# Performance work log

Measured on AMD Instinct MI355X. Metric: run time of the kernel, lower is better.

Reference implementation:

```python
import jax, jax.numpy as jnp
import numpy as np

N = 50000   # total nodes
D = 128     # feature dim
E = 800000  # edges (avg degree 16)
G = 100     # graphs (500 nodes each)


def setup_inputs() -> dict:
    key = jax.random.key(0)
    ks = jax.random.split(key, 9)
    s = 1.0 / np.sqrt(D)
    X = jax.random.normal(ks[0], (N, D), jnp.float32)
    src = jax.random.randint(ks[1], (E,), 0, N)
    dst = jax.random.randint(ks[2], (E,), 0, N)
    edge_index = jnp.stack([src, dst])  # [2, E]
    edge_weight = jax.random.uniform(ks[3], (E,), jnp.float32)
    # 100 graphs of 500 nodes each (graph_sizes = [500]*100)
    segment_ids = jnp.repeat(jnp.arange(G), N // G)
    return {
        "X": X,
        "edge_weight": edge_weight,
        "W1": jax.random.normal(ks[4], (D, D), jnp.float32) * s,
        "b1": jnp.zeros((D,), jnp.float32),
        "W2": jax.random.normal(ks[5], (D, D), jnp.float32) * s,
        "b2": jnp.zeros((D,), jnp.float32),
        "Wf": jax.random.normal(ks[6], (D, 1), jnp.float32) * s,
        "bf": jnp.zeros((1,), jnp.float32),
        "edge_index": edge_index,
        "segment_ids": segment_ids,
    }


def gcn_conv(X, edge_index, edge_weight, W, b):
    # h_v = sum_{(u->v)} w_e * (X @ W)[u] + b   (sparse A @ XW)
    h = X @ W                                   # [N, d_out]
    msgs = h[edge_index[0]] * edge_weight[:, None]  # [E, d_out]
    agg = jax.ops.segment_sum(msgs, edge_index[1], num_segments=N)
    return agg + b


def reference(X, edge_weight, W1, b1, W2, b2, Wf, bf, edge_index, segment_ids):
    # layer stack: conv -> relu -> dropout(eval=identity)
    h = jax.nn.relu(gcn_conv(X, edge_index, edge_weight, W1, b1))
    h = jax.nn.relu(gcn_conv(h, edge_index, edge_weight, W2, b2))
    out = jax.nn.sigmoid(gcn_conv(h, edge_index, edge_weight, Wf, bf))  # [N, 1]
    # fused per-graph mean readout (replaces split(graph_sizes) python loop)
    sums = jax.ops.segment_sum(out.sum(axis=1), segment_ids, num_segments=G)
    counts = jax.ops.segment_sum(jnp.ones((N,), out.dtype), segment_ids, num_segments=G)
    return sums / (counts * out.shape[1])  # [G]
```

## Files before the change

### kernel.cpp

```cpp
#include <hip/hip_runtime.h>
#include <hip/hip_fp16.h>

#define N_NODES 50000
#define DIM 128
#define NEDGE 800000
#define NGRAPH 100
#define NPG 500
#define NBUCKET 250
#define NPB 200
#define BCAP 4096
#define CHUNK 2048
#define EPT (CHUNK / 256)

typedef _Float16 f16x8 __attribute__((ext_vector_type(8)));
typedef float f32x4 __attribute__((ext_vector_type(4)));
typedef float f32x2 __attribute__((ext_vector_type(2)));

__device__ inline float wgt(unsigned p) {
    return __half2float(__ushort_as_half((unsigned short)(p & 0xffffu)));
}
__device__ inline void accrow(uint2 q, float w, float* acc) {
    f32x2 f;
    f = __builtin_amdgcn_cvt_pk_f32_fp8((int)q.x, false); acc[0] = fmaf(w, f[0], acc[0]); acc[1] = fmaf(w, f[1], acc[1]);
    f = __builtin_amdgcn_cvt_pk_f32_fp8((int)q.x, true);  acc[2] = fmaf(w, f[0], acc[2]); acc[3] = fmaf(w, f[1], acc[3]);
    f = __builtin_amdgcn_cvt_pk_f32_fp8((int)q.y, false); acc[4] = fmaf(w, f[0], acc[4]); acc[5] = fmaf(w, f[1], acc[5]);
    f = __builtin_amdgcn_cvt_pk_f32_fp8((int)q.y, true);  acc[6] = fmaf(w, f[0], acc[6]); acc[7] = fmaf(w, f[1], acc[7]);
}
__device__ inline unsigned pack_fp8x4(float a, float b, float c, float d) {
    int v = __builtin_amdgcn_cvt_pk_fp8_f32(a, b, 0, false);
    v = __builtin_amdgcn_cvt_pk_fp8_f32(c, d, v, true);
    return (unsigned)v;
}

__global__ void prep(const float* __restrict__ W1, const float* __restrict__ W2,
                     _Float16* __restrict__ fragW1, _Float16* __restrict__ fragW2,
                     int* __restrict__ gCur) {
    const int b = blockIdx.x;
    if (b == 128) {
        int t = threadIdx.x;
        if (t < NBUCKET) gCur[t] = t * BCAP;
        return;
    }
    const float* W = (b < 64) ? W1 : W2;
    _Float16* F = (b < 64) ? fragW1 : fragW2;
    int idx = (b & 63) * 256 + threadIdx.x;
    int j = idx & 7, l = (idx >> 3) & 63, kt = (idx >> 9) & 3, nt = idx >> 11;
    int k = kt * 32 + ((l >> 4) << 3) + j;
    int col = (nt << 4) + (l & 15);
    F[idx] = (_Float16)W[k * DIM + col];
}

__global__ void bucket_scatter(const int* __restrict__ src, const int* __restrict__ dst,
                               const float* __restrict__ w, int* __restrict__ gCur,
                               uint2* __restrict__ stage, int E) {
    __shared__ int hist[NBUCKET];
    __shared__ int base[NBUCKET];
    for (int i = threadIdx.x; i < NBUCKET; i += 256) hist[i] = 0;
    __syncthreads();
    const int e0 = blockIdx.x * CHUNK;
    int myDst[EPT];
#pragma unroll
    for (int j = 0; j < EPT; ++j) {
        int e = e0 + j * 256 + threadIdx.x;
        int d = (e < E) ? dst[e] : -1;
        myDst[j] = d;
        if (d >= 0) atomicAdd(&hist[d / NPB], 1);
    }
    __syncthreads();
    for (int i = threadIdx.x; i < NBUCKET; i += 256)
        base[i] = atomicAdd(&gCur[i], hist[i]);
    __syncthreads();
#pragma unroll
    for (int j = 0; j < EPT; ++j) {
        int d = myDst[j];
        if (d >= 0) {
            int e = e0 + j * 256 + threadIdx.x;
            int b = d / NPB;
            int p = atomicAdd(&base[b], 1);
            unsigned short wh = __half_as_ushort(__float2half_rn(w[e]));
            stage[p] = make_uint2(((unsigned)src[e] << 16) | (unsigned)wh,
                                  (unsigned)(d - b * NPB));
        }
    }
}

__device__ inline f16x8 load_afrag_f32(const float* a) {
    float4 u0 = *(const float4*)a;
    float4 u1 = *(const float4*)(a + 4);
    f16x8 r;
    r[0] = (_Float16)u0.x; r[1] = (_Float16)u0.y; r[2] = (_Float16)u0.z; r[3] = (_Float16)u0.w;
    r[4] = (_Float16)u1.x; r[5] = (_Float16)u1.y; r[6] = (_Float16)u1.z; r[7] = (_Float16)u1.w;
    return r;
}
__device__ inline f16x8 load_afrag_fp8(const unsigned char* a) {
    uint2 q = *(const uint2*)a;
    f32x2 f0 = __builtin_amdgcn_cvt_pk_f32_fp8((int)q.x, false);
    f32x2 f1 = __builtin_amdgcn_cvt_pk_f32_fp8((int)q.x, true);
    f32x2 f2 = __builtin_amdgcn_cvt_pk_f32_fp8((int)q.y, false);
    f32x2 f3 = __builtin_amdgcn_cvt_pk_f32_fp8((int)q.y, true);
    f16x8 r;
    r[0] = (_Float16)f0[0]; r[1] = (_Float16)f0[1]; r[2] = (_Float16)f1[0]; r[3] = (_Float16)f1[1];
    r[4] = (_Float16)f2[0]; r[5] = (_Float16)f2[1]; r[6] = (_Float16)f3[0]; r[7] = (_Float16)f3[1];
    return r;
}

template <typename TIN>
__device__ inline void gemm_tile(const TIN* __restrict__ A, const _Float16* fragW,
                                 unsigned char* __restrict__ C, int blk, int tid) {
    const int lane = tid & 63;
    const int wid = tid >> 6;
    const int row0 = blk * 128 + wid * 16;
    if (row0 >= N_NODES) return;
    const int arow = row0 + (lane & 15);
    const int koff = (lane >> 4) << 3;
    f32x4 acc[8] = {};
#pragma unroll
    for (int kt = 0; kt < 4; ++kt) {
        f16x8 a;
        const TIN* ap = A + (size_t)arow * DIM + kt * 32 + koff;
        if constexpr (sizeof(TIN) == 4) a = load_afrag_f32((const float*)ap);
        else                            a = load_afrag_fp8((const unsigned char*)ap);
#pragma unroll
        for (int nt = 0; nt < 8; ++nt) {
            f16x8 b = *(const f16x8*)&fragW[(((nt << 2) | kt) << 9) | (lane << 3)];
            acc[nt] = __builtin_amdgcn_mfma_f32_16x16x32_f16(a, b, acc[nt], 0, 0, 0);
        }
    }
    const int crow = row0 + ((lane >> 4) << 2);
    const int ccol = lane & 15;
#pragma unroll
    for (int nt = 0; nt < 8; ++nt) {
#pragma unroll
        for (int r = 0; r < 4; ++r) {
            int v8 = __builtin_amdgcn_cvt_pk_fp8_f32(acc[nt][r], acc[nt][r], 0, false);
            C[(size_t)(crow + r) * DIM + (nt << 4) + ccol] = (unsigned char)(v8 & 0xff);
        }
    }
}

template <typename TIN>
__global__ __launch_bounds__(512) void gemm_mfma(const TIN* __restrict__ A,
                                                 const _Float16* __restrict__ fragWg,
                                                 unsigned char* __restrict__ C) {
    __shared__ __align__(16) _Float16 fragW[16384];
    const int tid = threadIdx.x;
    for (int i = tid; i < 2048; i += 512)
        ((uint4*)fragW)[i] = ((const uint4*)fragWg)[i];
    __syncthreads();
    gemm_tile<TIN>(A, fragW, C, blockIdx.x, tid);
}

#define MFMA_BLK ((N_NODES + 127) / 128)
__global__ __launch_bounds__(512) void gemm1_build(
        const float* __restrict__ A, const _Float16* __restrict__ fragWg,
        unsigned char* __restrict__ C, const int* __restrict__ gCur,
        const uint2* __restrict__ stage, unsigned int* __restrict__ pack,
        int2* __restrict__ range) {
    __shared__ __align__(16) _Float16 fragW[16384];
    __shared__ int lhist[NPB];
    __shared__ int lincl[256];
    __shared__ int lcur[NPB];
    const int tid = threadIdx.x;
    if (blockIdx.x < MFMA_BLK) {
        for (int i = tid; i < 2048; i += 512)
            ((uint4*)fragW)[i] = ((const uint4*)fragWg)[i];
        __syncthreads();
        gemm_tile<float>(A, fragW, C, blockIdx.x, tid);
        return;
    }
    const int b = blockIdx.x - MFMA_BLK;
    const int t = tid;
    const int cnt = gCur[b] - b * BCAP;
    for (int i = t; i < NPB; i += 512) lhist[i] = 0;
    __syncthreads();
    unsigned myX[BCAP / 512];
    int myLd[BCAP / 512];
#pragma unroll
    for (int j = 0; j < BCAP / 512; ++j) {
        int i = j * 512 + t;
        if (i < cnt) {
            uint2 r = stage[b * BCAP + i];
            myX[j] = r.x;
            myLd[j] = (int)r.y;
            atomicAdd(&lhist[r.y], 1);
        } else {
            myLd[j] = -1;
        }
    }
    __syncthreads();
    int h = (t < NPB) ? lhist[t] : 0;
    if (t < 256) lincl[t] = h;
    __syncthreads();
    for (int off = 1; off < 256; off <<= 1) {
        int v = (t >= off && t < 256) ? lincl[t - off] : 0;
        __syncthreads();
        if (t < 256) lincl[t] += v;
        __syncthreads();
    }
    if (t < NPB) lcur[t] = lincl[t] - h;
    __syncthreads();
#pragma unroll
    for (int j = 0; j < BCAP / 512; ++j) {
        if (myLd[j] >= 0) {
            int p = atomicAdd(&lcur[myLd[j]], 1);
            pack[b * BCAP + p] = myX[j];
        }
    }
    if (t < NPB) {
        int v = b * NPB + t;
        range[v] = make_int2(b * BCAP + lincl[t] - h, b * BCAP + lincl[t]);
    }
}

template <int MODE>
__global__ void gather_feat(const unsigned char* __restrict__ msg,
                            const unsigned int* __restrict__ pack,
                            const int2* __restrict__ range, const float* __restrict__ bias,
                            const float* __restrict__ wf, unsigned char* __restrict__ outF,
                            float* __restrict__ outS) {
    int gid = blockIdx.x * blockDim.x + threadIdx.x;
    int grp = gid >> 4, lane = gid & 15;
    if (grp >= N_NODES) return;
    int2 r = range[grp];
    int beg = r.x, end = r.y;
    float acc[8] = {};
    int i = beg;
    for (; i + 7 < end; i += 8) {
        unsigned p[8];
        uint2 q[8];
#pragma unroll
        for (int j = 0; j < 8; ++j) p[j] = pack[i + j];
#pragma unroll
        for (int j = 0; j < 8; ++j)
            q[j] = ((const uint2*)(msg + (size_t)(p[j] >> 16) * DIM))[lane];
#pragma unroll
        for (int j = 0; j < 8; ++j) accrow(q[j], wgt(p[j]), acc);
    }
    for (; i + 3 < end; i += 4) {
        unsigned p0 = pack[i], p1 = pack[i + 1], p2 = pack[i + 2], p3 = pack[i + 3];
        uint2 q0 = ((const uint2*)(msg + (size_t)(p0 >> 16) * DIM))[lane];
        uint2 q1 = ((const uint2*)(msg + (size_t)(p1 >> 16) * DIM))[lane];
        uint2 q2 = ((const uint2*)(msg + (size_t)(p2 >> 16) * DIM))[lane];
        uint2 q3 = ((const uint2*)(msg + (size_t)(p3 >> 16) * DIM))[lane];
        accrow(q0, wgt(p0), acc);
        accrow(q1, wgt(p1), acc);
        accrow(q2, wgt(p2), acc);
        accrow(q3, wgt(p3), acc);
    }
    for (; i < end; ++i) {
        unsigned p = pack[i];
        uint2 q = ((const uint2*)(msg + (size_t)(p >> 16) * DIM))[lane];
        accrow(q, wgt(p), acc);
    }
    float4 b0 = ((const float4*)bias)[2 * lane];
    float4 b1 = ((const float4*)bias)[2 * lane + 1];
    acc[0] = fmaxf(acc[0] + b0.x, 0.f); acc[1] = fmaxf(acc[1] + b0.y, 0.f);
    acc[2] = fmaxf(acc[2] + b0.z, 0.f); acc[3] = fmaxf(acc[3] + b0.w, 0.f);
    acc[4] = fmaxf(acc[4] + b1.x, 0.f); acc[5] = fmaxf(acc[5] + b1.y, 0.f);
    acc[6] = fmaxf(acc[6] + b1.z, 0.f); acc[7] = fmaxf(acc[7] + b1.w, 0.f);
    if (MODE == 0) {
        uint2 o;
        o.x = pack_fp8x4(acc[0], acc[1], acc[2], acc[3]);
        o.y = pack_fp8x4(acc[4], acc[5], acc[6], acc[7]);
        ((uint2*)(outF + (size_t)grp * DIM))[lane] = o;
    } else {
        float4 f0 = ((const float4*)wf)[2 * lane];
        float4 f1 = ((const float4*)wf)[2 * lane + 1];
        float d = acc[0] * f0.x + acc[1] * f0.y + acc[2] * f0.z + acc[3] * f0.w
                + acc[4] * f1.x + acc[5] * f1.y + acc[6] * f1.z + acc[7] * f1.w;
#pragma unroll
        for (int off = 8; off; off >>= 1) d += __shfl_down(d, off, 16);
        if (lane == 0) outS[grp] = d;
    }
}

__global__ void final_readout(const float* __restrict__ s, const unsigned int* __restrict__ pack,
                              const int2* __restrict__ range, const float* __restrict__ bfp,
                              float* __restrict__ out) {
    __shared__ float red[256];
    int g = blockIdx.x;
    float bf = bfp[0];
    float sum = 0.f;
    for (int n = threadIdx.x; n < NPG; n += blockDim.x) {
        int v = g * NPG + n;
        int2 r = range[v];
        float a = 0.f;
        for (int i = r.x; i < r.y; ++i) {
            unsigned int p = pack[i];
            a += wgt(p) * s[p >> 16];
        }
        a += bf;
        sum += 1.f / (1.f + expf(-a));
    }
    red[threadIdx.x] = sum;
    __syncthreads();
    for (int t = 128; t > 0; t >>= 1) {
        if (threadIdx.x < t) red[threadIdx.x] += red[threadIdx.x + t];
        __syncthreads();
    }
    if (threadIdx.x == 0) out[g] = red[0] / (float)NPG;
}

extern "C" void kernel_launch(void* const* d_in, const int* in_sizes, int n_in,
                              void* d_out, int out_size, void* d_ws, size_t ws_size,
                              hipStream_t stream) {
    const float* X  = (const float*)d_in[0];
    const float* ew = (const float*)d_in[1];
    const float* W1 = (const float*)d_in[2];
    const float* b1 = (const float*)d_in[3];
    const float* W2 = (const float*)d_in[4];
    const float* b2 = (const float*)d_in[5];
    const float* Wf = (const float*)d_in[6];
    const float* bf = (const float*)d_in[7];
    const int* ei   = (const int*)d_in[8];
    const int* src  = ei;
    const int* dst  = ei + NEDGE;

    float* out = (float*)d_out;

    char* ws = (char*)d_ws;
    size_t off = 0;
    unsigned char* bufA = (unsigned char*)(ws + off); off += (size_t)N_NODES * DIM;
    unsigned char* bufB = (unsigned char*)(ws + off); off += (size_t)N_NODES * DIM;
    uint2* stage = (uint2*)(ws + off);  off += (size_t)NBUCKET * BCAP * 8;
    unsigned int* pack = (unsigned int*)(ws + off); off += (size_t)NBUCKET * BCAP * 4;
    int2* range = (int2*)(ws + off);    off += (size_t)N_NODES * 8;
    int* gCur   = (int*)(ws + off);     off += (size_t)256 * 4;
    _Float16* fragW1 = (_Float16*)(ws + off); off += (size_t)16384 * 2;
    _Float16* fragW2 = (_Float16*)(ws + off); off += (size_t)16384 * 2;
    float* s_node = (float*)(ws + off); off += (size_t)N_NODES * 4;

    const int TB = 256;
    const int SCAT_BLK = (NEDGE + CHUNK - 1) / CHUNK;
    const int GATHER_BLK = (N_NODES * 16 + TB - 1) / TB;

    prep<<<129, TB, 0, stream>>>(W1, W2, fragW1, fragW2, gCur);
    bucket_scatter<<<SCAT_BLK, TB, 0, stream>>>(src, dst, ew, gCur, stage, NEDGE);
    gemm1_build<<<MFMA_BLK + NBUCKET, 512, 0, stream>>>(X, fragW1, bufA, gCur,
                                                        stage, pack, range);
    gather_feat<0><<<GATHER_BLK, TB, 0, stream>>>(bufA, pack, range, b1,
                                                  nullptr, bufB, nullptr);
    gemm_mfma<unsigned char><<<MFMA_BLK, 512, 0, stream>>>(bufB, fragW2, bufA);
    gather_feat<1><<<GATHER_BLK, TB, 0, stream>>>(bufA, pack, range, b2,
                                                  Wf, nullptr, s_node);
    final_readout<<<NGRAPH, TB, 0, stream>>>(s_node, pack, range, bf, out);
}
```

Measured before the change: 106.9 us.

## Fuse layer-1 gather with layer-2 GEMM via shared-memory fp16 tile

Each 256-thread block now gathers 16 destination nodes for layer 1 and writes the bias+ReLU result as fp16 into a swizzled LDS tile. It then runs MFMA against W2 straight from that tile, with each of four waves producing two 16-column tiles. This removes a kernel launch, the fp8 round trip of the intermediate hidden features through global memory, and the fp8 dequant in the A-fragment load. The intermediate is now kept in fp16 rather than fp8, which changes precision slightly. fragW2 is read from global memory rather than staged in LDS, and each block does only a small GEMM.

```diff
diff --git a/kernel.cpp b/kernel.cpp
--- a/kernel.cpp
+++ b/kernel.cpp
@@ -92,21 +92,9 @@
     r[4] = (_Float16)u1.x; r[5] = (_Float16)u1.y; r[6] = (_Float16)u1.z; r[7] = (_Float16)u1.w;
     return r;
 }
-__device__ inline f16x8 load_afrag_fp8(const unsigned char* a) {
-    uint2 q = *(const uint2*)a;
-    f32x2 f0 = __builtin_amdgcn_cvt_pk_f32_fp8((int)q.x, false);
-    f32x2 f1 = __builtin_amdgcn_cvt_pk_f32_fp8((int)q.x, true);
-    f32x2 f2 = __builtin_amdgcn_cvt_pk_f32_fp8((int)q.y, false);
-    f32x2 f3 = __builtin_amdgcn_cvt_pk_f32_fp8((int)q.y, true);
-    f16x8 r;
-    r[0] = (_Float16)f0[0]; r[1] = (_Float16)f0[1]; r[2] = (_Float16)f1[0]; r[3] = (_Float16)f1[1];
-    r[4] = (_Float16)f2[0]; r[5] = (_Float16)f2[1]; r[6] = (_Float16)f3[0]; r[7] = (_Float16)f3[1];
-    return r;
-}
-
-template <typename TIN>
-__device__ inline void gemm_tile(const TIN* __restrict__ A, const _Float16* fragW,
-                                 unsigned char* __restrict__ C, int blk, int tid) {
+
+__device__ inline void gemm_tile_f32(const float* __restrict__ A, const _Float16* fragW,
+                                     unsigned char* __restrict__ C, int blk, int tid) {
     const int lane = tid & 63;
     const int wid = tid >> 6;
     const int row0 = blk * 128 + wid * 16;
@@ -116,10 +104,7 @@
     f32x4 acc[8] = {};
 #pragma unroll
     for (int kt = 0; kt < 4; ++kt) {
-        f16x8 a;
-        const TIN* ap = A + (size_t)arow * DIM + kt * 32 + koff;
-        if constexpr (sizeof(TIN) == 4) a = load_afrag_f32((const float*)ap);
-        else                            a = load_afrag_fp8((const unsigned char*)ap);
+        f16x8 a = load_afrag_f32(A + (size_t)arow * DIM + kt * 32 + koff);
 #pragma unroll
         for (int nt = 0; nt < 8; ++nt) {
             f16x8 b = *(const f16x8*)&fragW[(((nt << 2) | kt) << 9) | (lane << 3)];
@@ -136,18 +121,6 @@
             C[(size_t)(crow + r) * DIM + (nt << 4) + ccol] = (unsigned char)(v8 & 0xff);
         }
     }
-}
-
-template <typename TIN>
-__global__ __launch_bounds__(512) void gemm_mfma(const TIN* __restrict__ A,
-                                                 const _Float16* __restrict__ fragWg,
-                                                 unsigned char* __restrict__ C) {
-    __shared__ __align__(16) _Float16 fragW[16384];
-    const int tid = threadIdx.x;
-    for (int i = tid; i < 2048; i += 512)
-        ((uint4*)fragW)[i] = ((const uint4*)fragWg)[i];
-    __syncthreads();
-    gemm_tile<TIN>(A, fragW, C, blockIdx.x, tid);
 }
 
 #define MFMA_BLK ((N_NODES + 127) / 128)
@@ -165,7 +138,7 @@
         for (int i = tid; i < 2048; i += 512)
             ((uint4*)fragW)[i] = ((const uint4*)fragWg)[i];
         __syncthreads();
-        gemm_tile<float>(A, fragW, C, blockIdx.x, tid);
+        gemm_tile_f32(A, fragW, C, blockIdx.x, tid);
         return;
     }
     const int b = blockIdx.x - MFMA_BLK;
@@ -212,12 +185,93 @@
     }
 }
 
-template <int MODE>
-__global__ void gather_feat(const unsigned char* __restrict__ msg,
-                            const unsigned int* __restrict__ pack,
-                            const int2* __restrict__ range, const float* __restrict__ bias,
-                            const float* __restrict__ wf, unsigned char* __restrict__ outF,
-                            float* __restrict__ outS) {
+__global__ __launch_bounds__(256) void gather_gemm2(
+        const unsigned char* __restrict__ msg, const unsigned int* __restrict__ pack,
+        const int2* __restrict__ range, const float* __restrict__ bias,
+        const _Float16* __restrict__ fragW2, unsigned char* __restrict__ C) {
+    __shared__ __align__(16) char hT[16 * 256];
+    const int t = threadIdx.x;
+    const int grpL = t >> 4;
+    const int lane16 = t & 15;
+    const int tile = blockIdx.x;
+    {
+        const int grp = tile * 16 + grpL;
+        int2 r = range[grp];
+        int beg = r.x, end = r.y;
+        float acc[8] = {};
+        int i = beg;
+        for (; i + 7 < end; i += 8) {
+            unsigned p[8];
+            uint2 q[8];
+#pragma unroll
+            for (int j = 0; j < 8; ++j) p[j] = pack[i + j];
+#pragma unroll
+            for (int j = 0; j < 8; ++j)
+                q[j] = ((const uint2*)(msg + (size_t)(p[j] >> 16) * DIM))[lane16];
+#pragma unroll
+            for (int j = 0; j < 8; ++j) accrow(q[j], wgt(p[j]), acc);
+        }
+        for (; i + 3 < end; i += 4) {
+            unsigned p0 = pack[i], p1 = pack[i + 1], p2 = pack[i + 2], p3 = pack[i + 3];
+            uint2 q0 = ((const uint2*)(msg + (size_t)(p0 >> 16) * DIM))[lane16];
+            uint2 q1 = ((const uint2*)(msg + (size_t)(p1 >> 16) * DIM))[lane16];
+            uint2 q2 = ((const uint2*)(msg + (size_t)(p2 >> 16) * DIM))[lane16];
+            uint2 q3 = ((const uint2*)(msg + (size_t)(p3 >> 16) * DIM))[lane16];
+            accrow(q0, wgt(p0), acc);
+            accrow(q1, wgt(p1), acc);
+            accrow(q2, wgt(p2), acc);
+            accrow(q3, wgt(p3), acc);
+        }
+        for (; i < end; ++i) {
+            unsigned p = pack[i];
+            uint2 q = ((const uint2*)(msg + (size_t)(p >> 16) * DIM))[lane16];
+            accrow(q, wgt(p), acc);
+        }
+        float4 b0 = ((const float4*)bias)[2 * lane16];
+        float4 b1 = ((const float4*)bias)[2 * lane16 + 1];
+        union { __half2 h[4]; uint4 u; } o;
+        o.h[0] = __floats2half2_rn(fmaxf(acc[0] + b0.x, 0.f), fmaxf(acc[1] + b0.y, 0.f));
+        o.h[1] = __floats2half2_rn(fmaxf(acc[2] + b0.z, 0.f), fmaxf(acc[3] + b0.w, 0.f));
+        o.h[2] = __floats2half2_rn(fmaxf(acc[4] + b1.x, 0.f), fmaxf(acc[5] + b1.y, 0.f));
+        o.h[3] = __floats2half2_rn(fmaxf(acc[6] + b1.z, 0.f), fmaxf(acc[7] + b1.w, 0.f));
+        int boff = (grpL << 8) | (lane16 << 4);
+        boff ^= (grpL & 7) << 4;
+        *(uint4*)(hT + boff) = o.u;
+    }
+    __syncthreads();
+    const int lane = t & 63;
+    const int wid = t >> 6;
+    const int arowL = lane & 15;
+    const int koff = (lane >> 4) << 3;
+    f32x4 acc2[2] = {};
+#pragma unroll
+    for (int kt = 0; kt < 4; ++kt) {
+        int boff = (arowL << 8) | ((kt * 32 + koff) << 1);
+        boff ^= (arowL & 7) << 4;
+        f16x8 a = *(const f16x8*)(hT + boff);
+#pragma unroll
+        for (int n = 0; n < 2; ++n) {
+            int nt = wid * 2 + n;
+            f16x8 b = *(const f16x8*)&fragW2[(((nt << 2) | kt) << 9) | (lane << 3)];
+            acc2[n] = __builtin_amdgcn_mfma_f32_16x16x32_f16(a, b, acc2[n], 0, 0, 0);
+        }
+    }
+    const int crow = tile * 16 + ((lane >> 4) << 2);
+    const int ccol = lane & 15;
+#pragma unroll
+    for (int n = 0; n < 2; ++n) {
+#pragma unroll
+        for (int r = 0; r < 4; ++r) {
+            int v8 = __builtin_amdgcn_cvt_pk_fp8_f32(acc2[n][r], acc2[n][r], 0, false);
+            C[(size_t)(crow + r) * DIM + ((wid * 2 + n) << 4) + ccol] = (unsigned char)(v8 & 0xff);
+        }
+    }
+}
+
+__global__ void gather_wf(const unsigned char* __restrict__ msg,
+                          const unsigned int* __restrict__ pack,
+                          const int2* __restrict__ range, const float* __restrict__ bias,
+                          const float* __restrict__ wf, float* __restrict__ outS) {
     int gid = blockIdx.x * blockDim.x + threadIdx.x;
     int grp = gid >> 4, lane = gid & 15;
     if (grp >= N_NODES) return;
@@ -254,24 +308,15 @@
     }
     float4 b0 = ((const float4*)bias)[2 * lane];
     float4 b1 = ((const float4*)bias)[2 * lane + 1];
-    acc[0] = fmaxf(acc[0] + b0.x, 0.f); acc[1] = fmaxf(acc[1] + b0.y, 0.f);
-    acc[2] = fmaxf(acc[2] + b0.z, 0.f); acc[3] = fmaxf(acc[3] + b0.w, 0.f);
-    acc[4] = fmaxf(acc[4] + b1.x, 0.f); acc[5] = fmaxf(acc[5] + b1.y, 0.f);
-    acc[6] = fmaxf(acc[6] + b1.z, 0.f); acc[7] = fmaxf(acc[7] + b1.w, 0.f);
-    if (MODE == 0) {
-        uint2 o;
-        o.x = pack_fp8x4(acc[0], acc[1], acc[2], acc[3]);
-        o.y = pack_fp8x4(acc[4], acc[5], acc[6], acc[7]);
-        ((uint2*)(outF + (size_t)grp * DIM))[lane] = o;
-    } else {
-        float4 f0 = ((const float4*)wf)[2 * lane];
-        float4 f1 = ((const float4*)wf)[2 * lane + 1];
-        float d = acc[0] * f0.x + acc[1] * f0.y + acc[2] * f0.z + acc[3] * f0.w
-                + acc[4] * f1.x + acc[5] * f1.y + acc[6] * f1.z + acc[7] * f1.w;
-#pragma unroll
-        for (int off = 8; off; off >>= 1) d += __shfl_down(d, off, 16);
-        if (lane == 0) outS[grp] = d;
-    }
+    float4 f0 = ((const float4*)wf)[2 * lane];
+    float4 f1 = ((const float4*)wf)[2 * lane + 1];
+    float d = fmaxf(acc[0] + b0.x, 0.f) * f0.x + fmaxf(acc[1] + b0.y, 0.f) * f0.y
+            + fmaxf(acc[2] + b0.z, 0.f) * f0.z + fmaxf(acc[3] + b0.w, 0.f) * f0.w
+            + fmaxf(acc[4] + b1.x, 0.f) * f1.x + fmaxf(acc[5] + b1.y, 0.f) * f1.y
+            + fmaxf(acc[6] + b1.z, 0.f) * f1.z + fmaxf(acc[7] + b1.w, 0.f) * f1.w;
+#pragma unroll
+    for (int off = 8; off; off >>= 1) d += __shfl_down(d, off, 16);
+    if (lane == 0) outS[grp] = d;
 }
 
 __global__ void final_readout(const float* __restrict__ s, const unsigned int* __restrict__ pack,
@@ -332,16 +377,14 @@
 
     const int TB = 256;
     const int SCAT_BLK = (NEDGE + CHUNK - 1) / CHUNK;
+    const int TILE_BLK = N_NODES / 16;
     const int GATHER_BLK = (N_NODES * 16 + TB - 1) / TB;
 
     prep<<<129, TB, 0, stream>>>(W1, W2, fragW1, fragW2, gCur);
     bucket_scatter<<<SCAT_BLK, TB, 0, stream>>>(src, dst, ew, gCur, stage, NEDGE);
     gemm1_build<<<MFMA_BLK + NBUCKET, 512, 0, stream>>>(X, fragW1, bufA, gCur,
                                                         stage, pack, range);
-    gather_feat<0><<<GATHER_BLK, TB, 0, stream>>>(bufA, pack, range, b1,
-                                                  nullptr, bufB, nullptr);
-    gemm_mfma<unsigned char><<<MFMA_BLK, 512, 0, stream>>>(bufB, fragW2, bufA);
-    gather_feat<1><<<GATHER_BLK, TB, 0, stream>>>(bufA, pack, range, b2,
-                                                  Wf, nullptr, s_node);
+    gather_gemm2<<<TILE_BLK, TB, 0, stream>>>(bufA, pack, range, b1, fragW2, bufB);
+    gather_wf<<<GATHER_BLK, TB, 0, stream>>>(bufB, pack, range, b2, Wf, s_node);
     final_readout<<<NGRAPH, TB, 0, stream>>>(s_node, pack, range, bf, out);
 }
```

Result: faster. 99.02 us (-7.4%).
